# Performance work log

Measured on AMD Instinct MI355X. Metric: run time of the kernel, lower is better.

The kernel has to match this reference:

```python
import jax, jax.numpy as jnp
import numpy as np

KK_THRESHOLD = 1000.0

def setup_inputs() -> dict:
    key = jax.random.key(0)
    k1, k2 = jax.random.split(key)
    x = jax.random.normal(k1, (8192, 4096), dtype=jnp.float32)
    # kernel initialized Uniform(-0.1, 0.1) as in the original layer
    kernel = jax.random.uniform(k2, (4096, 4096), dtype=jnp.float32, minval=-0.1, maxval=0.1)
    bias = jnp.zeros((4096,), dtype=jnp.float32)
    nmk = jnp.float32(1.0)
    kk = jnp.float32(1.0)  # < 1000 -> soft tanh quantization branch
    return {"x": x, "kernel": kernel, "bias": bias, "nmk": nmk, "kk": kk}

def reference(x, kernel, bias, nmk, kk):
    def soft(_):
        # training-time soft binarization: tanh(kk * W)
        return nmk * jnp.matmul(x, jnp.tanh(kernel * kk)) + bias
    def hard(_):
        # fully binarized: sign(W)
        return nmk * jnp.matmul(x, jnp.sign(kernel)) + bias
    return jax.lax.cond(kk < KK_THRESHOLD, soft, hard, operand=None)
```

## Files before the change

kernel.cpp:

```cpp
#include <hip/hip_runtime.h>
#include <hip/hip_bf16.h>
#include <stdint.h>

typedef __bf16 bf16x8 __attribute__((ext_vector_type(8)));
typedef float f32x16 __attribute__((ext_vector_type(16)));
typedef unsigned int u32;
typedef __attribute__((address_space(1))) const u32 g_u32;
typedef __attribute__((address_space(3))) u32 l_u32;

__device__ __forceinline__ unsigned short f32_bf16_rne(float f) {
    unsigned u = __float_as_uint(f);
    u += 0x7FFFu + ((u >> 16) & 1u);
    return (unsigned short)(u >> 16);
}

__device__ __forceinline__ float fast_tanh(float z) {
    return 1.0f - 2.0f / (1.0f + __expf(2.0f * z));
}

__device__ __forceinline__ void lds16(const void* g, void* l) {
    __builtin_amdgcn_global_load_lds((g_u32*)g, (l_u32*)l, 16, 0, 0);
}

__global__ __launch_bounds__(256) void prep(
    const float* __restrict__ x, unsigned short* __restrict__ xb, int n8,
    const float* __restrict__ W, unsigned short* __restrict__ Wt,
    const float* __restrict__ kk_p, int K, int N, int qbx, int qblocks)
{
    const int t = threadIdx.x;
    if ((int)blockIdx.x < qblocks) {
        __shared__ unsigned short tileT[64][66];
        const float kk = *kk_p;
        const bool soft = kk < 1000.0f;
        const int nb = (blockIdx.x % qbx) * 64;
        const int kb = (blockIdx.x / qbx) * 64;
#pragma unroll
        for (int j = 0; j < 4; ++j) {
            const int r  = j * 16 + (t >> 4);
            const int c4 = (t & 15) * 4;
            float4 w = *(const float4*)&W[(size_t)(kb + r) * N + nb + c4];
            float q0, q1, q2, q3;
            if (soft) {
                q0 = fast_tanh(w.x * kk); q1 = fast_tanh(w.y * kk);
                q2 = fast_tanh(w.z * kk); q3 = fast_tanh(w.w * kk);
            } else {
                q0 = (w.x > 0.f) ? 1.f : (w.x < 0.f ? -1.f : 0.f);
                q1 = (w.y > 0.f) ? 1.f : (w.y < 0.f ? -1.f : 0.f);
                q2 = (w.z > 0.f) ? 1.f : (w.z < 0.f ? -1.f : 0.f);
                q3 = (w.w > 0.f) ? 1.f : (w.w < 0.f ? -1.f : 0.f);
            }
            tileT[c4 + 0][r] = f32_bf16_rne(q0);
            tileT[c4 + 1][r] = f32_bf16_rne(q1);
            tileT[c4 + 2][r] = f32_bf16_rne(q2);
            tileT[c4 + 3][r] = f32_bf16_rne(q3);
        }
        __syncthreads();
#pragma unroll
        for (int j = 0; j < 2; ++j) {
            const int n = j * 32 + (t >> 3);
            const int c = (t & 7) * 8;
            uint4 v;
            v.x = *(const u32*)&tileT[n][c + 0];
            v.y = *(const u32*)&tileT[n][c + 2];
            v.z = *(const u32*)&tileT[n][c + 4];
            v.w = *(const u32*)&tileT[n][c + 6];
            *(uint4*)&Wt[(size_t)(nb + n) * K + kb + c] = v;
        }
    } else {
        const int i = ((int)blockIdx.x - qblocks) * 256 + t;
        if (i >= n8) return;
        const float4* p = (const float4*)x + (size_t)i * 2;
        float4 a = p[0];
        float4 b = p[1];
        union { unsigned short u[8]; uint4 v; } o;
        o.u[0] = f32_bf16_rne(a.x); o.u[1] = f32_bf16_rne(a.y);
        o.u[2] = f32_bf16_rne(a.z); o.u[3] = f32_bf16_rne(a.w);
        o.u[4] = f32_bf16_rne(b.x); o.u[5] = f32_bf16_rne(b.y);
        o.u[6] = f32_bf16_rne(b.z); o.u[7] = f32_bf16_rne(b.w);
        *((uint4*)xb + i) = o.v;
    }
}

__global__ __launch_bounds__(256) void gemm_bf16_bt(
    const unsigned short* __restrict__ A,
    const unsigned short* __restrict__ Bt,
    const float* __restrict__ bias,
    const float* __restrict__ nmk_p,
    float* __restrict__ C,
    int M, int N, int K)
{
    __shared__ __align__(16) unsigned short As[128 * 32];
    __shared__ __align__(16) unsigned short Bs[128 * 32];

    const int tid  = threadIdx.x;
    const int wave = tid >> 6;
    const int lane = tid & 63;
    const int mTile = blockIdx.y * 128;
    const int nTile = blockIdx.x * 128;
    const int wm = (wave & 1) * 64;
    const int wn = (wave >> 1) * 64;
    const int lm = lane & 31;
    const int half = lane >> 5;

    f32x16 acc[2][2] = {};

    const int srow = tid >> 2;
    const int scol = (((tid & 3) ^ ((srow >> 1) & 3))) * 8;
    const unsigned short* Ag0 = A  + (size_t)(mTile + srow) * K + scol;
    const unsigned short* Ag1 = Ag0 + (size_t)64 * K;
    const unsigned short* Bg0 = Bt + (size_t)(nTile + srow) * K + scol;
    const unsigned short* Bg1 = Bg0 + (size_t)64 * K;

    char* asw = (char*)As + wave * 1024;
    char* bsw = (char*)Bs + wave * 1024;

    const int g = (lane >> 1) & 3;
    const int p0 = (half ^ g) * 16;

    for (int k0 = 0; k0 < K; k0 += 32) {
        __syncthreads();
        lds16(Ag0, asw);
        lds16(Ag1, asw + 4096);
        lds16(Bg0, bsw);
        lds16(Bg1, bsw + 4096);
        Ag0 += 32; Ag1 += 32; Bg0 += 32; Bg1 += 32;
        __syncthreads();

        bf16x8 af[2][2], bf[2][2];
#pragma unroll
        for (int mi = 0; mi < 2; ++mi) {
            const int rb = (wm + 32 * mi + lm) * 64;
            af[mi][0] = *(const bf16x8*)((const char*)As + rb + p0);
            af[mi][1] = *(const bf16x8*)((const char*)As + rb + (p0 ^ 32));
        }
#pragma unroll
        for (int ni = 0; ni < 2; ++ni) {
            const int rb = (wn + 32 * ni + lm) * 64;
            bf[ni][0] = *(const bf16x8*)((const char*)Bs + rb + p0);
            bf[ni][1] = *(const bf16x8*)((const char*)Bs + rb + (p0 ^ 32));
        }
#pragma unroll
        for (int ks = 0; ks < 2; ++ks)
#pragma unroll
            for (int mi = 0; mi < 2; ++mi)
#pragma unroll
                for (int ni = 0; ni < 2; ++ni)
                    acc[mi][ni] = __builtin_amdgcn_mfma_f32_32x32x16_bf16(
                        af[mi][ks], bf[ni][ks], acc[mi][ni], 0, 0, 0);
    }

    const float nmk = *nmk_p;
    float bn[2];
#pragma unroll
    for (int ni = 0; ni < 2; ++ni) bn[ni] = bias[nTile + wn + 32 * ni + lm];

#pragma unroll
    for (int mi = 0; mi < 2; ++mi) {
        const int mbase = mTile + wm + 32 * mi + 4 * half;
#pragma unroll
        for (int ni = 0; ni < 2; ++ni) {
            const int n = nTile + wn + 32 * ni + lm;
#pragma unroll
            for (int reg = 0; reg < 16; ++reg) {
                const int row = mbase + (reg & 3) + 8 * (reg >> 2);
                C[(size_t)row * N + n] = nmk * acc[mi][ni][reg] + bn[ni];
            }
        }
    }
}

__global__ void fallback_gemm(const float* __restrict__ x, const float* __restrict__ W,
                              const float* __restrict__ bias, const float* __restrict__ nmk_p,
                              const float* __restrict__ kk_p, float* __restrict__ C,
                              int M, int N, int K) {
    __shared__ float At[16][17];
    __shared__ float Bq[16][17];
    const int tx = threadIdx.x, ty = threadIdx.y;
    const int n = blockIdx.x * 16 + tx;
    const int m = blockIdx.y * 16 + ty;
    const float kk = *kk_p;
    const bool soft = kk < 1000.f;
    float acc = 0.f;
    for (int k0 = 0; k0 < K; k0 += 16) {
        At[ty][tx] = x[(size_t)m * K + k0 + tx];
        float w = W[(size_t)(k0 + ty) * N + n];
        Bq[ty][tx] = soft ? tanhf(w * kk) : (w > 0.f ? 1.f : (w < 0.f ? -1.f : 0.f));
        __syncthreads();
#pragma unroll
        for (int kk2 = 0; kk2 < 16; ++kk2) acc += At[ty][kk2] * Bq[kk2][tx];
        __syncthreads();
    }
    C[(size_t)m * N + n] = (*nmk_p) * acc + bias[n];
}

extern "C" void kernel_launch(void* const* d_in, const int* in_sizes, int n_in,
                              void* d_out, int out_size, void* d_ws, size_t ws_size,
                              hipStream_t stream) {
    const float* x    = (const float*)d_in[0];
    const float* W    = (const float*)d_in[1];
    const float* bias = (const float*)d_in[2];
    const float* nmk  = (const float*)d_in[3];
    const float* kk   = (const float*)d_in[4];
    float* out = (float*)d_out;

    const int N = in_sizes[2];
    const int K = in_sizes[1] / N;
    const int M = in_sizes[0] / K;

    const size_t need = ((size_t)M * K + (size_t)N * K) * sizeof(unsigned short);
    const bool shapes_ok = (M % 128 == 0) && (N % 128 == 0) && (K % 64 == 0) &&
                           (N % 64 == 0) && ((M * K) % 2048 == 0);

    if (ws_size >= need && shapes_ok) {
        unsigned short* xb = (unsigned short*)d_ws;
        unsigned short* Wt = xb + (size_t)M * K;

        const int n8 = (M * K) / 8;
        const int qbx = N / 64;
        const int qblocks = qbx * (K / 64);
        const int cblocks = (n8 + 255) / 256;
        prep<<<qblocks + cblocks, 256, 0, stream>>>(x, xb, n8, W, Wt, kk, K, N, qbx, qblocks);

        dim3 gg(N / 128, M / 128);
        gemm_bf16_bt<<<gg, 256, 0, stream>>>(xb, Wt, bias, nmk, out, M, N, K);
    } else {
        dim3 fg(N / 16, M / 16);
        fallback_gemm<<<fg, dim3(16, 16), 0, stream>>>(x, W, bias, nmk, kk, out, M, N, K);
    }
}
```

Baseline: 592.5 us.

## Rewrite GEMM with 256x256 tiles, double-buffered LDS pipeline and XCD-aware remap

Measured after the change: 486.9 us. 1.22x faster.

```diff
diff --git a/kernel.cpp b/kernel.cpp
--- a/kernel.cpp
+++ b/kernel.cpp
@@ -3,7 +3,7 @@
 #include <stdint.h>
 
 typedef __bf16 bf16x8 __attribute__((ext_vector_type(8)));
-typedef float f32x16 __attribute__((ext_vector_type(16)));
+typedef float f32x4 __attribute__((ext_vector_type(4)));
 typedef unsigned int u32;
 typedef __attribute__((address_space(1))) const u32 g_u32;
 typedef __attribute__((address_space(3))) u32 l_u32;
@@ -81,7 +81,7 @@
     }
 }
 
-__global__ __launch_bounds__(256) void gemm_bf16_bt(
+__global__ __launch_bounds__(512, 2) void gemm_bf16_256(
     const unsigned short* __restrict__ A,
     const unsigned short* __restrict__ Bt,
     const float* __restrict__ bias,
@@ -89,84 +89,149 @@
     float* __restrict__ C,
     int M, int N, int K)
 {
-    __shared__ __align__(16) unsigned short As[128 * 32];
-    __shared__ __align__(16) unsigned short Bs[128 * 32];
+    __shared__ __align__(16) char lds[131072];
 
     const int tid  = threadIdx.x;
     const int wave = tid >> 6;
     const int lane = tid & 63;
-    const int mTile = blockIdx.y * 128;
-    const int nTile = blockIdx.x * 128;
-    const int wm = (wave & 1) * 64;
-    const int wn = (wave >> 1) * 64;
-    const int lm = lane & 31;
-    const int half = lane >> 5;
-
-    f32x16 acc[2][2] = {};
-
-    const int srow = tid >> 2;
-    const int scol = (((tid & 3) ^ ((srow >> 1) & 3))) * 8;
-    const unsigned short* Ag0 = A  + (size_t)(mTile + srow) * K + scol;
-    const unsigned short* Ag1 = Ag0 + (size_t)64 * K;
-    const unsigned short* Bg0 = Bt + (size_t)(nTile + srow) * K + scol;
-    const unsigned short* Bg1 = Bg0 + (size_t)64 * K;
-
-    char* asw = (char*)As + wave * 1024;
-    char* bsw = (char*)Bs + wave * 1024;
-
-    const int g = (lane >> 1) & 3;
-    const int p0 = (half ^ g) * 16;
-
-    for (int k0 = 0; k0 < K; k0 += 32) {
-        __syncthreads();
-        lds16(Ag0, asw);
-        lds16(Ag1, asw + 4096);
-        lds16(Bg0, bsw);
-        lds16(Bg1, bsw + 4096);
-        Ag0 += 32; Ag1 += 32; Bg0 += 32; Bg1 += 32;
-        __syncthreads();
-
-        bf16x8 af[2][2], bf[2][2];
-#pragma unroll
-        for (int mi = 0; mi < 2; ++mi) {
-            const int rb = (wm + 32 * mi + lm) * 64;
-            af[mi][0] = *(const bf16x8*)((const char*)As + rb + p0);
-            af[mi][1] = *(const bf16x8*)((const char*)As + rb + (p0 ^ 32));
-        }
-#pragma unroll
-        for (int ni = 0; ni < 2; ++ni) {
-            const int rb = (wn + 32 * ni + lm) * 64;
-            bf[ni][0] = *(const bf16x8*)((const char*)Bs + rb + p0);
-            bf[ni][1] = *(const bf16x8*)((const char*)Bs + rb + (p0 ^ 32));
-        }
-#pragma unroll
-        for (int ks = 0; ks < 2; ++ks)
-#pragma unroll
-            for (int mi = 0; mi < 2; ++mi)
-#pragma unroll
-                for (int ni = 0; ni < 2; ++ni)
-                    acc[mi][ni] = __builtin_amdgcn_mfma_f32_32x32x16_bf16(
-                        af[mi][ks], bf[ni][ks], acc[mi][ni], 0, 0, 0);
+    const int wr = wave >> 2;
+    const int wc = wave & 3;
+
+    const int nbx = N >> 8;
+    const int nwg = (int)gridDim.x;
+    int id = (int)blockIdx.x;
+    {
+        const int xcd = id & 7, lid = id >> 3;
+        const int q8 = nwg >> 3, r8 = nwg & 7;
+        id = (xcd < r8 ? xcd * (q8 + 1) : r8 * (q8 + 1) + (xcd - r8) * q8) + lid;
+    }
+    const int mTile = (id / nbx) << 8;
+    const int nTile = (id % nbx) << 8;
+
+    const size_t Kb = (size_t)K * 2;
+    const char* pA[2];
+    const char* pB[2];
+#pragma unroll
+    for (int q = 0; q < 2; ++q) {
+        const int s  = (wave * 2 + q) * 64 + lane;
+        const int g  = s >> 6;
+        const int r4 = (s >> 2) & 15;
+        const int c4 = (s & 3) ^ ((r4 >> 1) & 3);
+        const int row = ((g >> 1) << 4) + r4;
+        const int cb  = (((g & 1) << 2) + c4) << 4;
+        pA[q] = (const char*)A  + (size_t)(mTile + row) * Kb + cb;
+        pB[q] = (const char*)Bt + (size_t)(nTile + row) * Kb + cb;
+    }
+    const size_t HSTEP = (size_t)128 * Kb;
+    const int w2k = wave * 2048;
+
+    const int laneoff = ((lane & 15) << 6)
+                      + ((((lane >> 4) ^ (((lane & 15) >> 1) & 3))) << 4);
+
+    f32x4 acc[8][4] = {};
+    const int NT = K >> 6;
+
+#define STG_A(buf, t, h) do {                                                  \
+    char* _d = lds + (buf) * 65536 + (h) * 16384 + w2k;                        \
+    lds16(pA[0] + (size_t)(h) * HSTEP + (size_t)(t) * 128, _d);                \
+    lds16(pA[1] + (size_t)(h) * HSTEP + (size_t)(t) * 128, _d + 1024);         \
+} while (0)
+#define STG_B(buf, t, h) do {                                                  \
+    char* _d = lds + 32768 + (buf) * 65536 + (h) * 16384 + w2k;                \
+    lds16(pB[0] + (size_t)(h) * HSTEP + (size_t)(t) * 128, _d);                \
+    lds16(pB[1] + (size_t)(h) * HSTEP + (size_t)(t) * 128, _d + 1024);         \
+} while (0)
+#define LDA(dst, buf, mi, ks) dst = *(const bf16x8*)(lds + (buf) * 65536       \
+        + ((wr * 8 + (mi)) * 2048) + (ks) * 1024 + laneoff)
+#define LDB(dst, buf, ni, ks) dst = *(const bf16x8*)(lds + 32768               \
+        + (buf) * 65536 + ((wc * 4 + (ni)) * 2048) + (ks) * 1024 + laneoff)
+#define BAR() __builtin_amdgcn_s_barrier()
+#define LGKM0() asm volatile("s_waitcnt lgkmcnt(0)" ::: "memory")
+#define MFMA_Q(p)                                                              \
+    __builtin_amdgcn_s_setprio(1);                                             \
+    { _Pragma("unroll")                                                        \
+      for (int ii = 0; ii < 2; ++ii) {                                         \
+        _Pragma("unroll")                                                      \
+        for (int ni = 0; ni < 4; ++ni) {                                       \
+          _Pragma("unroll")                                                    \
+          for (int ks = 0; ks < 2; ++ks)                                       \
+            acc[2 * (p) + ii][ni] = __builtin_amdgcn_mfma_f32_16x16x32_bf16(   \
+                af[ii][ks], bf[ni][ks], acc[2 * (p) + ii][ni], 0, 0, 0);       \
+        } } }                                                                  \
+    __builtin_amdgcn_s_setprio(0)
+
+    STG_A(0, 0, 0); STG_A(0, 0, 1);
+    STG_B(0, 0, 0); STG_B(0, 0, 1);
+    STG_B(1, 1, 0); STG_B(1, 1, 1);
+    asm volatile("s_waitcnt vmcnt(4)" ::: "memory");
+    BAR();
+
+    bf16x8 af[2][2], bf[4][2];
+
+    for (int t = 0; t < NT; ++t) {
+        const int buf = t & 1;
+        const int tA = (t + 1 < NT) ? (t + 1) : 0;
+        int tB = t + 2; if (tB >= NT) tB -= NT;
+
+        LDB(bf[0][0], buf, 0, 0); LDB(bf[0][1], buf, 0, 1);
+        LDB(bf[1][0], buf, 1, 0); LDB(bf[1][1], buf, 1, 1);
+        LDB(bf[2][0], buf, 2, 0); LDB(bf[2][1], buf, 2, 1);
+        LDB(bf[3][0], buf, 3, 0); LDB(bf[3][1], buf, 3, 1);
+        LDA(af[0][0], buf, 0, 0); LDA(af[0][1], buf, 0, 1);
+        LDA(af[1][0], buf, 1, 0); LDA(af[1][1], buf, 1, 1);
+        STG_A(buf ^ 1, tA, 0);
+        BAR(); LGKM0();
+        MFMA_Q(0);
+        BAR();
+
+        LDA(af[0][0], buf, 2, 0); LDA(af[0][1], buf, 2, 1);
+        LDA(af[1][0], buf, 3, 0); LDA(af[1][1], buf, 3, 1);
+        STG_A(buf ^ 1, tA, 1);
+        BAR(); LGKM0();
+        MFMA_Q(1);
+        BAR();
+
+        LDA(af[0][0], buf, 4, 0); LDA(af[0][1], buf, 4, 1);
+        LDA(af[1][0], buf, 5, 0); LDA(af[1][1], buf, 5, 1);
+        STG_B(buf, tB, 0);
+        BAR(); LGKM0();
+        MFMA_Q(2);
+        BAR();
+
+        LDA(af[0][0], buf, 6, 0); LDA(af[0][1], buf, 6, 1);
+        LDA(af[1][0], buf, 7, 0); LDA(af[1][1], buf, 7, 1);
+        STG_B(buf, tB, 1);
+        asm volatile("s_waitcnt vmcnt(4)" ::: "memory");
+        BAR(); LGKM0();
+        MFMA_Q(3);
+        BAR();
     }
 
     const float nmk = *nmk_p;
-    float bn[2];
-#pragma unroll
-    for (int ni = 0; ni < 2; ++ni) bn[ni] = bias[nTile + wn + 32 * ni + lm];
-
-#pragma unroll
-    for (int mi = 0; mi < 2; ++mi) {
-        const int mbase = mTile + wm + 32 * mi + 4 * half;
-#pragma unroll
-        for (int ni = 0; ni < 2; ++ni) {
-            const int n = nTile + wn + 32 * ni + lm;
-#pragma unroll
-            for (int reg = 0; reg < 16; ++reg) {
-                const int row = mbase + (reg & 3) + 8 * (reg >> 2);
-                C[(size_t)row * N + n] = nmk * acc[mi][ni][reg] + bn[ni];
+    const int l15 = lane & 15, lh = lane >> 4;
+    float bn[4];
+#pragma unroll
+    for (int ni = 0; ni < 4; ++ni) bn[ni] = bias[nTile + wc * 64 + ni * 16 + l15];
+
+#pragma unroll
+    for (int mi = 0; mi < 8; ++mi) {
+        const int rbase = mTile + wr * 128 + mi * 16 + lh * 4;
+#pragma unroll
+        for (int ni = 0; ni < 4; ++ni) {
+            const int col = nTile + wc * 64 + ni * 16 + l15;
+#pragma unroll
+            for (int reg = 0; reg < 4; ++reg) {
+                C[(size_t)(rbase + reg) * N + col] = nmk * acc[mi][ni][reg] + bn[ni];
             }
         }
     }
+#undef STG_A
+#undef STG_B
+#undef LDA
+#undef LDB
+#undef BAR
+#undef LGKM0
+#undef MFMA_Q
 }
 
 __global__ void fallback_gemm(const float* __restrict__ x, const float* __restrict__ W,
@@ -208,8 +273,8 @@
     const int M = in_sizes[0] / K;
 
     const size_t need = ((size_t)M * K + (size_t)N * K) * sizeof(unsigned short);
-    const bool shapes_ok = (M % 128 == 0) && (N % 128 == 0) && (K % 64 == 0) &&
-                           (N % 64 == 0) && ((M * K) % 2048 == 0);
+    const bool shapes_ok = (M % 256 == 0) && (N % 256 == 0) && (K % 64 == 0) &&
+                           (K >= 128) && ((M * K) % 2048 == 0);
 
     if (ws_size >= need && shapes_ok) {
         unsigned short* xb = (unsigned short*)d_ws;
@@ -221,8 +286,8 @@
         const int cblocks = (n8 + 255) / 256;
         prep<<<qblocks + cblocks, 256, 0, stream>>>(x, xb, n8, W, Wt, kk, K, N, qbx, qblocks);
 
-        dim3 gg(N / 128, M / 128);
-        gemm_bf16_bt<<<gg, 256, 0, stream>>>(xb, Wt, bias, nmk, out, M, N, K);
+        const int nwg = (M / 256) * (N / 256);
+        gemm_bf16_256<<<nwg, 512, 0, stream>>>(xb, Wt, bias, nmk, out, M, N, K);
     } else {
         dim3 fg(N / 16, M / 16);
         fallback_gemm<<<fg, dim3(16, 16), 0, stream>>>(x, W, bias, nmk, kk, out, M, N, K);
```
